# Performance work log

Measured on AMD Instinct MI355X. Metric: run time of the kernel, lower is better.

Reference implementation:

```python
import jax, jax.numpy as jnp
import numpy as np

# YOLOv3 COCO anchors (pixels); layer_no=1 -> stride 16; masked_anchors = ALL anchors / stride
ANCHORS = np.array([[10,13],[16,30],[33,23],[30,61],[62,45],[59,119],[116,90],[156,198],[373,326]], dtype=np.float32)
STRIDE = 16.0
N_ANCHORS = 9
N_CLASSES = 80
N_CH = 5 + N_CLASSES  # 85


def setup_inputs() -> dict:
    key = jax.random.key(0)
    k1, k2, k3 = jax.random.split(key, 3)
    B, C, H, W = 16, 256, 64, 64
    xin = jax.random.normal(k1, (B, C, H, W), jnp.float32)
    conv_w = jax.random.normal(k2, (N_ANCHORS * N_CH, C), jnp.float32) * 0.02  # 1x1 conv kernel
    conv_b = jnp.zeros((N_ANCHORS * N_CH,), jnp.float32)
    prior_labels = jax.random.uniform(k3, (16, 50, 5), jnp.float32)  # [class,xc,yc,w,h] in [0,1]
    return {"xin": xin, "conv_w": conv_w, "conv_b": conv_b, "prior_labels": prior_labels}


def reference(xin, conv_w, conv_b, prior_labels):
    # Inference branch of YOLOimgLayer.forward (labels=None): decode + return pred.
    # prior_labels is consumed in the torch forward (truth_i/j indices) but unused on this path.
    B, C, H, W = xin.shape
    fsize = H
    # 1x1 conv == channel-mixing matmul
    out = jnp.einsum('bchw,oc->bohw', xin, conv_w) + conv_b[None, :, None, None]
    # (B, A, n_ch, H, W) -> (B, A, H, W, n_ch)
    out = out.reshape(B, N_ANCHORS, N_CH, fsize, fsize).transpose(0, 1, 3, 4, 2)
    # sigmoid channels [0:2] (x,y) and [4:] (obj + classes); leave w,h raw
    ch = jnp.arange(N_CH)
    sig_mask = (ch < 2) | (ch >= 4)
    out = jnp.where(sig_mask, jax.nn.sigmoid(out), out)

    anchors_g = jnp.asarray(ANCHORS / STRIDE, dtype=xin.dtype)  # (A, 2) grid units
    w_a = anchors_g[:, 0][None, :, None, None]  # broadcast over (B, A, H, W)
    h_a = anchors_g[:, 1][None, :, None, None]
    x_shift = jnp.arange(fsize, dtype=xin.dtype)[None, None, None, :]  # varies along W
    y_shift = jnp.arange(fsize, dtype=xin.dtype)[None, None, :, None]  # varies along H

    px = ((out[..., 0] - 0.5) * w_a + x_shift) * STRIDE
    py = ((out[..., 1] - 0.5) * h_a + y_shift) * STRIDE
    pw = jnp.exp(out[..., 2]) * w_a * STRIDE
    ph = jnp.exp(out[..., 3]) * h_a * STRIDE

    pred = jnp.concatenate(
        [px[..., None], py[..., None], pw[..., None], ph[..., None], out[..., 4:]], axis=-1
    )  # (B, A, H, W, 85)
    return pred
```

## Files before the change

### kernel.cpp

```cpp
#include <hip/hip_runtime.h>

typedef __attribute__((ext_vector_type(8))) short bf16x8;
typedef __attribute__((ext_vector_type(4))) float f32x4;
typedef __attribute__((ext_vector_type(4))) int i32x4;
typedef __attribute__((ext_vector_type(4))) unsigned short u16x4;

#define KDIM 256
#define HWSZ 4096
#define NOUT 765
#define NOUTP 768

__constant__ float c_AW[10] = {10.f,16.f,33.f,30.f,62.f,59.f,116.f,156.f,373.f,0.f};
__constant__ float c_AH[10] = {13.f,30.f,23.f,61.f,45.f,119.f,90.f,198.f,326.f,0.f};

__device__ __forceinline__ unsigned short f2bf(float f) {
  unsigned u = __builtin_bit_cast(unsigned, f);
  u += 0x7fffu + ((u >> 16) & 1u);
  return (unsigned short)(u >> 16);
}

__device__ __forceinline__ float sigf(float t) {
  return 1.0f / (1.0f + __expf(-t));
}

__global__ void prep_w(const float* __restrict__ cw, unsigned short* __restrict__ wbf) {
  int e = (blockIdx.x * 256 + threadIdx.x) * 4;
  int o = e >> 8, col = e & 255;
  f32x4 v = {0.f, 0.f, 0.f, 0.f};
  if (o < NOUT) v = *reinterpret_cast<const f32x4*>(cw + o * KDIM + col);
  u16x4 u = { f2bf(v.x), f2bf(v.y), f2bf(v.z), f2bf(v.w) };
  *reinterpret_cast<u16x4*>(wbf + e) = u;
}

__global__ __launch_bounds__(512, 2) void yolo_main(
    const float* __restrict__ xin,
    const unsigned short* __restrict__ wbf,
    const float* __restrict__ bias,
    float* __restrict__ out)
{
  __shared__ __align__(16) unsigned short xT[64 * KDIM];

  const int b    = blockIdx.x >> 6;
  const int pc   = blockIdx.x & 63;
  const int tid  = threadIdx.x;
  const int lane = tid & 63;
  const int wv   = tid >> 6;

  {
    const float* xsrc = xin + ((size_t)b * KDIM) * HWSZ + pc * 64;
    const int p  = lane;
    const int sw = (p & 7) << 3;
    #pragma unroll
    for (int i = 0; i < 4; ++i) {
      const int c0 = (wv + 8 * i) << 3;
      float v[8];
      #pragma unroll
      for (int j = 0; j < 8; ++j) v[j] = xsrc[(size_t)(c0 + j) * HWSZ + p];
      union { i32x4 q; unsigned short us[8]; } pk;
      #pragma unroll
      for (int j = 0; j < 8; ++j) pk.us[j] = f2bf(v[j]);
      *reinterpret_cast<i32x4*>(&xT[(p << 8) + (c0 ^ sw)]) = pk.q;
    }
  }
  __syncthreads();

  const int g     = lane >> 4;
  const int r16   = lane & 15;
  const int obase = wv * 96;

  f32x4 acc[6][4];
  #pragma unroll
  for (int ot = 0; ot < 6; ++ot)
    #pragma unroll
    for (int pt = 0; pt < 4; ++pt)
      acc[ot][pt] = f32x4{0.f, 0.f, 0.f, 0.f};

  const unsigned short* wptr = wbf + (size_t)(obase + r16) * KDIM + 8 * g;

  #pragma unroll
  for (int kk = 0; kk < 8; ++kk) {
    bf16x8 xfr[4];
    #pragma unroll
    for (int pt = 0; pt < 4; ++pt) {
      const int pxl = pt * 16 + r16;
      const int e   = (pxl << 8) + ((kk * 32 + 8 * g) ^ ((pxl & 7) << 3));
      xfr[pt] = __builtin_bit_cast(bf16x8, *reinterpret_cast<const i32x4*>(&xT[e]));
    }
    #pragma unroll
    for (int ot = 0; ot < 6; ++ot) {
      bf16x8 wfr = __builtin_bit_cast(bf16x8,
          *reinterpret_cast<const i32x4*>(wptr + ot * 16 * KDIM + kk * 32));
      #pragma unroll
      for (int pt = 0; pt < 4; ++pt)
        acc[ot][pt] = __builtin_amdgcn_mfma_f32_16x16x32_bf16(xfr[pt], wfr, acc[ot][pt], 0, 0, 0);
    }
  }

  const float ys = (float)pc * 16.0f;
  #pragma unroll
  for (int ot = 0; ot < 6; ++ot) {
    const int o = obase + ot * 16 + r16;
    int a = o / 85;
    const int ch = o - a * 85;
    if (a > 8) a = 8;
    const bool valid = (o < NOUT);
    const float aw = c_AW[a], ah = c_AH[a];
    const float bi = valid ? bias[o] : 0.0f;
    #pragma unroll
    for (int pt = 0; pt < 4; ++pt) {
      #pragma unroll
      for (int r = 0; r < 4; ++r) {
        const int   pxl = pt * 16 + g * 4 + r;
        const float t   = acc[ot][pt][r] + bi;
        float val;
        if (ch >= 4)      val = sigf(t);
        else if (ch == 0) val = (sigf(t) - 0.5f) * aw + (float)pxl * 16.0f;
        else if (ch == 1) val = (sigf(t) - 0.5f) * ah + ys;
        else if (ch == 2) val = __expf(t) * aw;
        else              val = __expf(t) * ah;
        if (valid) {
          const size_t addr = (((size_t)(b * 9 + a) * HWSZ) + (size_t)(pc * 64 + pxl)) * 85 + ch;
          out[addr] = val;
        }
      }
    }
  }
}

extern "C" void kernel_launch(void* const* d_in, const int* in_sizes, int n_in,
                              void* d_out, int out_size, void* d_ws, size_t ws_size,
                              hipStream_t stream) {
  const float* xin = (const float*)d_in[0];
  const float* cw  = (const float*)d_in[1];
  const float* cb  = (const float*)d_in[2];
  float* out = (float*)d_out;
  unsigned short* wbf = (unsigned short*)d_ws;

  prep_w<<<dim3((NOUTP * KDIM / 4) / 256), dim3(256), 0, stream>>>(cw, wbf);
  yolo_main<<<dim3(16 * 64), dim3(512), 0, stream>>>(xin, wbf, cb, out);
}
```

Baseline: 143.7 us.

## Persistent 16-pixel tiles with double-buffered input prefetch and LDS-staged coalesced stores

The main kernel now runs 512 blocks that each loop over 8 units of 16 pixels, instead of 1024 blocks that each handle 64 pixels. Each iteration prefetches the next unit's input into registers and writes it to a second LDS buffer, so loads overlap with the MFMA work. Results go to an LDS staging buffer in output layout and are written back as contiguous float4 stores, replacing the scattered stride-85 scalar stores. The cost is fewer MFMAs per weight-fragment load, more barriers per block, and a larger LDS footprint that may reduce occupancy.

```diff
diff --git a/kernel.cpp b/kernel.cpp
--- a/kernel.cpp
+++ b/kernel.cpp
@@ -9,9 +9,10 @@
 #define HWSZ 4096
 #define NOUT 765
 #define NOUTP 768
+#define UPB 8
 
-__constant__ float c_AW[10] = {10.f,16.f,33.f,30.f,62.f,59.f,116.f,156.f,373.f,0.f};
-__constant__ float c_AH[10] = {13.f,30.f,23.f,61.f,45.f,119.f,90.f,198.f,326.f,0.f};
+__constant__ float c_AW[9] = {10.f,16.f,33.f,30.f,62.f,59.f,116.f,156.f,373.f};
+__constant__ float c_AH[9] = {13.f,30.f,23.f,61.f,45.f,119.f,90.f,198.f,326.f};
 
 __device__ __forceinline__ unsigned short f2bf(float f) {
   unsigned u = __builtin_bit_cast(unsigned, f);
@@ -23,6 +24,12 @@
   return 1.0f / (1.0f + __expf(-t));
 }
 
+__device__ __forceinline__ void bar_lds() {
+  asm volatile("s_waitcnt lgkmcnt(0)" ::: "memory");
+  __builtin_amdgcn_s_barrier();
+  __builtin_amdgcn_sched_barrier(0);
+}
+
 __global__ void prep_w(const float* __restrict__ cw, unsigned short* __restrict__ wbf) {
   int e = (blockIdx.x * 256 + threadIdx.x) * 4;
   int o = e >> 8, col = e & 255;
@@ -32,98 +39,139 @@
   *reinterpret_cast<u16x4*>(wbf + e) = u;
 }
 
-__global__ __launch_bounds__(512, 2) void yolo_main(
+__global__ __launch_bounds__(512) void yolo_main(
     const float* __restrict__ xin,
     const unsigned short* __restrict__ wbf,
     const float* __restrict__ bias,
     float* __restrict__ out)
 {
-  __shared__ __align__(16) unsigned short xT[64 * KDIM];
+  __shared__ __align__(16) unsigned short xT[2][16 * 256];
+  __shared__ __align__(16) float stg[9 * 16 * 85];
 
-  const int b    = blockIdx.x >> 6;
-  const int pc   = blockIdx.x & 63;
   const int tid  = threadIdx.x;
   const int lane = tid & 63;
   const int wv   = tid >> 6;
+  const int g    = lane >> 4;
+  const int r16  = lane & 15;
+  const int obase = wv * 96;
+
+  const int u0 = blockIdx.x * UPB;
+  const int b  = u0 >> 8;
+
+  const int spx = tid & 15;
+  const int sck = tid >> 4;
+  const int sxe = spx * 256 + ((sck * 8) ^ ((spx & 7) << 3));
+  const float* xsb = xin + (size_t)b * (KDIM * HWSZ);
+
+  float aw6[6], ah6[6], bi6[6];
+  int   sof[6], och[6];
+  #pragma unroll
+  for (int ot = 0; ot < 6; ++ot) {
+    const int o  = obase + ot * 16 + r16;
+    const int a  = o / 85;
+    const int ch = o - a * 85;
+    och[ot] = ch;
+    const int ac = a < 9 ? a : 8;
+    aw6[ot] = c_AW[ac]; ah6[ot] = c_AH[ac];
+    bi6[ot] = bias[o < NOUT ? o : 0];
+    sof[ot] = a < 9 ? a * 1360 + ch : -1;
+  }
+  unsigned cOff[6];
+  #pragma unroll
+  for (int m = 0; m < 6; ++m) {
+    const int qq = tid + 512 * m;
+    const int a  = qq / 340;
+    cOff[m] = (unsigned)a * (HWSZ * 85u) + (unsigned)(qq - a * 340) * 4u;
+  }
+
+  const unsigned short* wp0 = wbf + (unsigned)(obase + r16) * KDIM + 8 * g;
 
   {
-    const float* xsrc = xin + ((size_t)b * KDIM) * HWSZ + pc * 64;
-    const int p  = lane;
-    const int sw = (p & 7) << 3;
+    const int py = (u0 >> 2) & 63, q = u0 & 3;
+    const float* xs = xsb + py * 64 + q * 16 + spx;
+    float v[8];
     #pragma unroll
-    for (int i = 0; i < 4; ++i) {
-      const int c0 = (wv + 8 * i) << 3;
-      float v[8];
+    for (int j = 0; j < 8; ++j) v[j] = xs[(size_t)(sck * 8 + j) * HWSZ];
+    union { i32x4 qv; unsigned short us[8]; } pk;
+    #pragma unroll
+    for (int j = 0; j < 8; ++j) pk.us[j] = f2bf(v[j]);
+    *reinterpret_cast<i32x4*>(&xT[0][sxe]) = pk.qv;
+  }
+  bar_lds();
+
+  float pf[8];
+  #pragma unroll 1
+  for (int i = 0; i < UPB; ++i) {
+    const int u  = u0 + i;
+    const int py = (u >> 2) & 63, q = u & 3;
+
+    if (i + 1 < UPB) {
+      const int un = u + 1;
+      const int pyn = (un >> 2) & 63, qn = un & 3;
+      const float* xs = xsb + pyn * 64 + qn * 16 + spx;
       #pragma unroll
-      for (int j = 0; j < 8; ++j) v[j] = xsrc[(size_t)(c0 + j) * HWSZ + p];
-      union { i32x4 q; unsigned short us[8]; } pk;
+      for (int j = 0; j < 8; ++j) pf[j] = xs[(size_t)(sck * 8 + j) * HWSZ];
+    }
+
+    f32x4 acc[6];
+    #pragma unroll
+    for (int ot = 0; ot < 6; ++ot) acc[ot] = f32x4{0.f, 0.f, 0.f, 0.f};
+    const unsigned short* xb = &xT[i & 1][0];
+    const int kxor = (r16 & 7) << 3;
+    #pragma unroll
+    for (int kk = 0; kk < 8; ++kk) {
+      const int ke = (kk * 32 + 8 * g) ^ kxor;
+      bf16x8 x0 = __builtin_bit_cast(bf16x8,
+          *reinterpret_cast<const i32x4*>(&xb[r16 * 256 + ke]));
       #pragma unroll
-      for (int j = 0; j < 8; ++j) pk.us[j] = f2bf(v[j]);
-      *reinterpret_cast<i32x4*>(&xT[(p << 8) + (c0 ^ sw)]) = pk.q;
+      for (int ot = 0; ot < 6; ++ot) {
+        bf16x8 w = __builtin_bit_cast(bf16x8,
+            *reinterpret_cast<const i32x4*>(wp0 + ot * (16 * KDIM) + kk * 32));
+        acc[ot] = __builtin_amdgcn_mfma_f32_16x16x32_bf16(x0, w, acc[ot], 0, 0, 0);
+      }
     }
-  }
-  __syncthreads();
 
-  const int g     = lane >> 4;
-  const int r16   = lane & 15;
-  const int obase = wv * 96;
-
-  f32x4 acc[6][4];
-  #pragma unroll
-  for (int ot = 0; ot < 6; ++ot)
-    #pragma unroll
-    for (int pt = 0; pt < 4; ++pt)
-      acc[ot][pt] = f32x4{0.f, 0.f, 0.f, 0.f};
-
-  const unsigned short* wptr = wbf + (size_t)(obase + r16) * KDIM + 8 * g;
-
-  #pragma unroll
-  for (int kk = 0; kk < 8; ++kk) {
-    bf16x8 xfr[4];
-    #pragma unroll
-    for (int pt = 0; pt < 4; ++pt) {
-      const int pxl = pt * 16 + r16;
-      const int e   = (pxl << 8) + ((kk * 32 + 8 * g) ^ ((pxl & 7) << 3));
-      xfr[pt] = __builtin_bit_cast(bf16x8, *reinterpret_cast<const i32x4*>(&xT[e]));
-    }
+    const float ys  = (float)py * 16.0f;
+    const float xs0 = (float)(q * 16) * 16.0f;
     #pragma unroll
     for (int ot = 0; ot < 6; ++ot) {
-      bf16x8 wfr = __builtin_bit_cast(bf16x8,
-          *reinterpret_cast<const i32x4*>(wptr + ot * 16 * KDIM + kk * 32));
-      #pragma unroll
-      for (int pt = 0; pt < 4; ++pt)
-        acc[ot][pt] = __builtin_amdgcn_mfma_f32_16x16x32_bf16(xfr[pt], wfr, acc[ot][pt], 0, 0, 0);
-    }
-  }
-
-  const float ys = (float)pc * 16.0f;
-  #pragma unroll
-  for (int ot = 0; ot < 6; ++ot) {
-    const int o = obase + ot * 16 + r16;
-    int a = o / 85;
-    const int ch = o - a * 85;
-    if (a > 8) a = 8;
-    const bool valid = (o < NOUT);
-    const float aw = c_AW[a], ah = c_AH[a];
-    const float bi = valid ? bias[o] : 0.0f;
-    #pragma unroll
-    for (int pt = 0; pt < 4; ++pt) {
-      #pragma unroll
-      for (int r = 0; r < 4; ++r) {
-        const int   pxl = pt * 16 + g * 4 + r;
-        const float t   = acc[ot][pt][r] + bi;
-        float val;
-        if (ch >= 4)      val = sigf(t);
-        else if (ch == 0) val = (sigf(t) - 0.5f) * aw + (float)pxl * 16.0f;
-        else if (ch == 1) val = (sigf(t) - 0.5f) * ah + ys;
-        else if (ch == 2) val = __expf(t) * aw;
-        else              val = __expf(t) * ah;
-        if (valid) {
-          const size_t addr = (((size_t)(b * 9 + a) * HWSZ) + (size_t)(pc * 64 + pxl)) * 85 + ch;
-          out[addr] = val;
+      if (sof[ot] >= 0) {
+        const int ch = och[ot];
+        float* sd = stg + sof[ot];
+        #pragma unroll
+        for (int r = 0; r < 4; ++r) {
+          const int   px = g * 4 + r;
+          const float tv = acc[ot][r] + bi6[ot];
+          float val;
+          if (ch >= 4)      val = sigf(tv);
+          else if (ch == 0) val = (sigf(tv) - 0.5f) * aw6[ot] + xs0 + (float)px * 16.0f;
+          else if (ch == 1) val = (sigf(tv) - 0.5f) * ah6[ot] + ys;
+          else if (ch == 2) val = __expf(tv) * aw6[ot];
+          else              val = __expf(tv) * ah6[ot];
+          sd[px * 85] = val;
         }
       }
     }
+    bar_lds();
+
+    {
+      float* outu = out + (size_t)b * (9u * HWSZ * 85u)
+                        + (unsigned)((py * 64 + q * 16) * 85);
+      #pragma unroll
+      for (int m = 0; m < 6; ++m) {
+        if (m < 5 || tid < 500) {
+          const f32x4 v = *reinterpret_cast<const f32x4*>(stg + (tid + 512 * m) * 4);
+          *reinterpret_cast<f32x4*>(outu + cOff[m]) = v;
+        }
+      }
+    }
+    if (i + 1 < UPB) {
+      union { i32x4 qv; unsigned short us[8]; } pk;
+      #pragma unroll
+      for (int j = 0; j < 8; ++j) pk.us[j] = f2bf(pf[j]);
+      *reinterpret_cast<i32x4*>(&xT[(i + 1) & 1][sxe]) = pk.qv;
+    }
+    bar_lds();
   }
 }
 
@@ -137,5 +185,5 @@
   unsigned short* wbf = (unsigned short*)d_ws;
 
   prep_w<<<dim3((NOUTP * KDIM / 4) / 256), dim3(256), 0, stream>>>(cw, wbf);
-  yolo_main<<<dim3(16 * 64), dim3(512), 0, stream>>>(xin, wbf, cb, out);
+  yolo_main<<<dim3(512), dim3(512), 0, stream>>>(xin, wbf, cb, out);
 }
```

New measurement: 246.9 us. 1.72x slower.
